# Performance work log

Measured on AMD Instinct MI355X. Metric: run time of the kernel, lower is better.

The kernel has to match this reference:

```python
import jax, jax.numpy as jnp
from jax import lax
import numpy as np

# sym6 reconstruction low-pass (pywt Wavelet('sym6').filter_bank[2]), length 12
SYM6_REC = [-0.007800708325034148, 0.0017677118642428036, 0.04472490177066578,
            -0.021060292512300564, -0.07263752278646252, 0.3379294217276218,
            0.787641141030194, 0.4910559419267466, -0.048311742585633,
            -0.11799011114819057, 0.0034907120842174702, 0.015404109327027373]

UP, DOWN = 1, 2
PAD = (len(SYM6_REC) - UP) // 2  # = 5


def setup_inputs() -> dict:
    key = jax.random.key(0)
    h = jnp.asarray(SYM6_REC, dtype=jnp.float32)
    kernel = h[None, :] * h[:, None]  # [12, 12] separable outer product
    x = jax.random.normal(key, (16, 64, 256, 256), dtype=jnp.float32)
    return {"input": x, "kernel": kernel}


def reference(input, kernel):
    # upfirdn2d: zero-insert upsample (lhs_dilation), pad, FIR convolve
    # (true convolution => flip kernel for lax correlation), strided downsample.
    B, C, H, W = input.shape
    w = jnp.flip(kernel, (0, 1))[None, None]        # [1, 1, kh, kw]
    x = input.reshape(B * C, 1, H, W)               # depthwise via batch fold
    y = lax.conv_general_dilated(
        x, w,
        window_strides=(DOWN, DOWN),
        padding=[(PAD, PAD), (PAD, PAD)],
        lhs_dilation=(UP, UP),
        dimension_numbers=('NCHW', 'OIHW', 'NCHW'))
    return y.reshape(B, C, y.shape[-2], y.shape[-1])
```

## Files before the change

kernel.cpp:

```cpp
#include <hip/hip_runtime.h>


#define H_IN  256
#define W_IN  256
#define H_OUT 128
#define W_OUT 128
#define KTAP  12
#define VSTR  276
#define FG    68
#define NTHR  256

typedef float f32x4 __attribute__((ext_vector_type(4)));

__global__ __launch_bounds__(NTHR)
void upfirdn2d_sym6(const float* __restrict__ x,
                    const float* __restrict__ k2d,
                    float* __restrict__ out) {
    __shared__ float vs[32 * VSTR];
    __shared__ float rsum[KTAP];

    const int tid = threadIdx.x;

    if (tid < KTAP) {
        const float4* kp = reinterpret_cast<const float4*>(k2d + 12 * tid);
        float4 a = kp[0], b = kp[1], c = kp[2];
        rsum[tid] = ((a.x + a.y) + (a.z + a.w))
                  + ((b.x + b.y) + (b.z + b.w))
                  + ((c.x + c.y) + (c.z + c.w));
    }
    __syncthreads();
    float w[KTAP];
    {
        float tot = 0.f;
        #pragma unroll
        for (int q = 0; q < KTAP; ++q) tot += rsum[q];
        const float r = rsqrtf(tot);
        #pragma unroll
        for (int p = 0; p < KTAP; ++p) w[p] = rsum[KTAP - 1 - p] * r;
    }

    const int bid = blockIdx.x;
    const int nb  = (bid & 7) * 512 + (bid >> 3);
    const int img = nb >> 2;
    const int ti  = nb & 3;

    const float* xim = x + (size_t)img * (H_IN * W_IN);
    float* oim = out + (size_t)img * (H_OUT * W_OUT);

    if (tid < 136) {
        const int rg  = tid / FG;
        const int cg  = tid - rg * FG;
        const int col = -8 + 4 * cg;
        const bool colok = (unsigned)col < (unsigned)W_IN;
        const int i0  = 16 * rg;
        const int gr0 = 64 * ti + 32 * rg - 5;

        float4 acc[16];
        #pragma unroll
        for (int k = 0; k < 16; ++k) acc[k] = make_float4(0.f, 0.f, 0.f, 0.f);

        const float* rp = xim + (size_t)gr0 * W_IN + col;
        #pragma unroll
        for (int rr = 0; rr < 42; ++rr) {
            const int gr = gr0 + rr;
            float4 v = make_float4(0.f, 0.f, 0.f, 0.f);
            if (colok && (unsigned)gr < (unsigned)H_IN)
                v = *reinterpret_cast<const float4*>(rp);
            rp += W_IN;
            #pragma unroll
            for (int ri = 0; ri < 16; ++ri) {
                const int p = rr - 2 * ri;
                if (p >= 0 && p < KTAP) {
                    acc[ri].x = fmaf(w[p], v.x, acc[ri].x);
                    acc[ri].y = fmaf(w[p], v.y, acc[ri].y);
                    acc[ri].z = fmaf(w[p], v.z, acc[ri].z);
                    acc[ri].w = fmaf(w[p], v.w, acc[ri].w);
                }
            }
        }
        #pragma unroll
        for (int ri = 0; ri < 16; ++ri)
            *reinterpret_cast<float4*>(&vs[(i0 + ri) * VSTR + 4 * cg]) = acc[ri];
    }
    __syncthreads();

    for (int t = tid; t < 512; t += NTHR) {
        const int i = t >> 4;
        const int g = t & 15;

        float f[32];
        #pragma unroll
        for (int m = 0; m < 8; ++m) {
            float4 v4 = *reinterpret_cast<const float4*>(&vs[i * VSTR + 16 * g + 4 * m]);
            f[4*m+0] = v4.x; f[4*m+1] = v4.y; f[4*m+2] = v4.z; f[4*m+3] = v4.w;
        }
        float o[8];
        #pragma unroll
        for (int jj = 0; jj < 8; ++jj) {
            float a = 0.f;
            #pragma unroll
            for (int q = 0; q < KTAP; ++q)
                a = fmaf(w[q], f[2*jj + 3 + q], a);
            o[jj] = a;
        }
        const int orow = 32 * ti + i;
        const int ocol = 8 * g;
        f32x4 o0 = { o[0], o[1], o[2], o[3] };
        f32x4 o1 = { o[4], o[5], o[6], o[7] };
        float* dst = oim + (size_t)orow * W_OUT + ocol;
        __builtin_nontemporal_store(o0, reinterpret_cast<f32x4*>(dst));
        __builtin_nontemporal_store(o1, reinterpret_cast<f32x4*>(dst + 4));
    }
}

extern "C" void kernel_launch(void* const* d_in, const int* in_sizes, int n_in,
                              void* d_out, int out_size, void* d_ws, size_t ws_size,
                              hipStream_t stream) {
    const float* x   = (const float*)d_in[0];
    const float* k2d = (const float*)d_in[1];
    float* out       = (float*)d_out;

    dim3 grid(4096);
    dim3 block(NTHR);
    upfirdn2d_sym6<<<grid, block, 0, stream>>>(x, k2d, out);
}
```

Before: 62.90 us.

## Double output rows per block and reuse overlapping input rows in registers

Each block now covers 64 output rows (half an image) instead of 32, and the grid is halved. Each vertical-pass thread processes two consecutive 16-row output chunks and keeps the 10 overlapping input rows in registers, so it does not reload them. This cuts the redundant halo reads of global memory. In exchange it doubles the LDS tile (about 70KB per block), which lowers occupancy, and it leaves fewer blocks to keep the GPU busy.

```diff
diff --git a/kernel.cpp b/kernel.cpp
--- a/kernel.cpp
+++ b/kernel.cpp
@@ -16,7 +16,7 @@
 void upfirdn2d_sym6(const float* __restrict__ x,
                     const float* __restrict__ k2d,
                     float* __restrict__ out) {
-    __shared__ float vs[32 * VSTR];
+    __shared__ float vs[64 * VSTR];
     __shared__ float rsum[KTAP];
 
     const int tid = threadIdx.x;
@@ -40,51 +40,89 @@
     }
 
     const int bid = blockIdx.x;
-    const int nb  = (bid & 7) * 512 + (bid >> 3);
-    const int img = nb >> 2;
-    const int ti  = nb & 3;
+    const int nb  = (bid & 7) * 256 + (bid >> 3);
+    const int img = nb >> 1;
+    const int ti  = nb & 1;
 
     const float* xim = x + (size_t)img * (H_IN * W_IN);
     float* oim = out + (size_t)img * (H_OUT * W_OUT);
 
     if (tid < 136) {
-        const int rg  = tid / FG;
-        const int cg  = tid - rg * FG;
+        const int sg  = tid / FG;
+        const int cg  = tid - sg * FG;
         const int col = -8 + 4 * cg;
         const bool colok = (unsigned)col < (unsigned)W_IN;
-        const int i0  = 16 * rg;
-        const int gr0 = 64 * ti + 32 * rg - 5;
-
-        float4 acc[16];
-        #pragma unroll
-        for (int k = 0; k < 16; ++k) acc[k] = make_float4(0.f, 0.f, 0.f, 0.f);
+        const int gr0 = 128 * ti + 64 * sg - 5;
+        const int lr0 = 32 * sg;
 
         const float* rp = xim + (size_t)gr0 * W_IN + col;
-        #pragma unroll
-        for (int rr = 0; rr < 42; ++rr) {
-            const int gr = gr0 + rr;
-            float4 v = make_float4(0.f, 0.f, 0.f, 0.f);
-            if (colok && (unsigned)gr < (unsigned)H_IN)
-                v = *reinterpret_cast<const float4*>(rp);
-            rp += W_IN;
+        float4 sv[10];
+
+        {
+            float4 acc[16];
             #pragma unroll
-            for (int ri = 0; ri < 16; ++ri) {
-                const int p = rr - 2 * ri;
-                if (p >= 0 && p < KTAP) {
-                    acc[ri].x = fmaf(w[p], v.x, acc[ri].x);
-                    acc[ri].y = fmaf(w[p], v.y, acc[ri].y);
-                    acc[ri].z = fmaf(w[p], v.z, acc[ri].z);
-                    acc[ri].w = fmaf(w[p], v.w, acc[ri].w);
+            for (int k = 0; k < 16; ++k) acc[k] = make_float4(0.f, 0.f, 0.f, 0.f);
+
+            #pragma unroll
+            for (int rr = 0; rr < 42; ++rr) {
+                const int gr = gr0 + rr;
+                float4 v = make_float4(0.f, 0.f, 0.f, 0.f);
+                if (colok && (unsigned)gr < (unsigned)H_IN)
+                    v = *reinterpret_cast<const float4*>(rp);
+                rp += W_IN;
+                if (rr >= 32) sv[rr - 32] = v;
+                #pragma unroll
+                for (int ri = 0; ri < 16; ++ri) {
+                    const int p = rr - 2 * ri;
+                    if (p >= 0 && p < KTAP) {
+                        acc[ri].x = fmaf(w[p], v.x, acc[ri].x);
+                        acc[ri].y = fmaf(w[p], v.y, acc[ri].y);
+                        acc[ri].z = fmaf(w[p], v.z, acc[ri].z);
+                        acc[ri].w = fmaf(w[p], v.w, acc[ri].w);
+                    }
                 }
             }
+            #pragma unroll
+            for (int ri = 0; ri < 16; ++ri)
+                *reinterpret_cast<float4*>(&vs[(lr0 + ri) * VSTR + 4 * cg]) = acc[ri];
         }
-        #pragma unroll
-        for (int ri = 0; ri < 16; ++ri)
-            *reinterpret_cast<float4*>(&vs[(i0 + ri) * VSTR + 4 * cg]) = acc[ri];
+
+        {
+            float4 acc[16];
+            #pragma unroll
+            for (int k = 0; k < 16; ++k) acc[k] = make_float4(0.f, 0.f, 0.f, 0.f);
+
+            #pragma unroll
+            for (int rr2 = 0; rr2 < 42; ++rr2) {
+                const int gr = gr0 + 32 + rr2;
+                float4 v;
+                if (rr2 < 10) {
+                    v = sv[rr2];
+                } else {
+                    v = make_float4(0.f, 0.f, 0.f, 0.f);
+                    if (colok && (unsigned)gr < (unsigned)H_IN)
+                        v = *reinterpret_cast<const float4*>(rp);
+                    rp += W_IN;
+                }
+                #pragma unroll
+                for (int ri = 0; ri < 16; ++ri) {
+                    const int p = rr2 - 2 * ri;
+                    if (p >= 0 && p < KTAP) {
+                        acc[ri].x = fmaf(w[p], v.x, acc[ri].x);
+                        acc[ri].y = fmaf(w[p], v.y, acc[ri].y);
+                        acc[ri].z = fmaf(w[p], v.z, acc[ri].z);
+                        acc[ri].w = fmaf(w[p], v.w, acc[ri].w);
+                    }
+                }
+            }
+            #pragma unroll
+            for (int ri = 0; ri < 16; ++ri)
+                *reinterpret_cast<float4*>(&vs[(lr0 + 16 + ri) * VSTR + 4 * cg]) = acc[ri];
+        }
     }
     __syncthreads();
 
-    for (int t = tid; t < 512; t += NTHR) {
+    for (int t = tid; t < 1024; t += NTHR) {
         const int i = t >> 4;
         const int g = t & 15;
 
@@ -103,7 +141,7 @@
                 a = fmaf(w[q], f[2*jj + 3 + q], a);
             o[jj] = a;
         }
-        const int orow = 32 * ti + i;
+        const int orow = 64 * ti + i;
         const int ocol = 8 * g;
         f32x4 o0 = { o[0], o[1], o[2], o[3] };
         f32x4 o1 = { o[4], o[5], o[6], o[7] };
@@ -120,7 +158,7 @@
     const float* k2d = (const float*)d_in[1];
     float* out       = (float*)d_out;
 
-    dim3 grid(4096);
+    dim3 grid(2048);
     dim3 block(NTHR);
     upfirdn2d_sym6<<<grid, block, 0, stream>>>(x, k2d, out);
 }
```

New measurement: 60.92 us (median of 2 runs). -3.2%, faster.
